# Optimization experiments

Hardware: AMD Instinct MI355X
Metric: run time of the kernel (lower is better)

Reference implementation:

```python
import jax, jax.numpy as jnp
import numpy as np

B, N, D = 4, 512, 128
NEG = -1e9


def setup_inputs() -> dict:
    key = jax.random.key(0)
    ks = jax.random.split(key, 11)
    s = 1.0 / np.sqrt(D)
    inp = {
        "q": jax.random.normal(ks[0], (B, N, D), jnp.float32),
        "k": jax.random.normal(ks[1], (B, N, D), jnp.float32),
        "v": jax.random.normal(ks[2], (B, N, D), jnp.float32),
        "mask": jnp.ones((B, N), jnp.int32),
        # nn.Linear params: weight [out,in], bias [out]
        "Wq": jax.random.uniform(ks[3], (D, D), jnp.float32, -s, s),
        "bq": jax.random.uniform(ks[4], (D,), jnp.float32, -s, s),
        "Wk": jax.random.uniform(ks[5], (D, D), jnp.float32, -s, s),
        "bk": jax.random.uniform(ks[6], (D,), jnp.float32, -s, s),
        "Wv": jax.random.uniform(ks[7], (D, D), jnp.float32, -s, s),
        "bv": jax.random.uniform(ks[8], (D,), jnp.float32, -s, s),
        "Wo": jax.random.uniform(ks[9], (D, D), jnp.float32, -s, s),
        "bo": jax.random.uniform(ks[10], (D,), jnp.float32, -s, s),
    }
    return inp


def reference(q, k, v, mask, Wq, bq, Wk, bk, Wv, bv, Wo, bo):
    # linear projections (torch Linear: x @ W.T + b)
    qp = jnp.einsum('bnd,ed->bne', q, Wq) + bq
    kp = jnp.einsum('bnd,ed->bne', k, Wk) + bk
    vp = jnp.einsum('bnd,ed->bne', v, Wv) + bv
    # outer-product attention: scores [b, n, m, d]
    scores = jnp.einsum('bnd,bmd->bnmd', qp, kp)
    # mask [b, n] -> [b, n, 1, 1], fill masked positions with -1e9
    scores = jnp.where(mask[:, :, None, None] == 0, NEG, scores)
    # per-channel softmax over m (axis=2); dropout is a no-op at inference
    scores = jax.nn.softmax(scores, axis=2)
    out = jnp.einsum('bnmd,bmd->bnd', scores, vp)
    return jnp.einsum('bnd,ed->bne', out, Wo) + bo
```

## Files before the change

kernel.cpp:

```cpp
#include <hip/hip_runtime.h>

#define BB 4
#define NN 512
#define DD 128

static constexpr float LOG2E = 1.4426950408889634f;
#define EXP2F(x) __builtin_amdgcn_exp2f(x)

__global__ __launch_bounds__(256) void wtrans_kernel(
    const float* __restrict__ Wq, const float* __restrict__ Wk,
    const float* __restrict__ Wv, const float* __restrict__ Wo,
    float* __restrict__ WTp)
{
    const int l = blockIdx.x * 256 + threadIdx.x;
    const int t = l >> 14;
    const int e = (l >> 7) & (DD - 1);
    const int j = l & (DD - 1);
    const float* W = (t == 0) ? Wq : (t == 1) ? Wk : (t == 2) ? Wv : Wo;
    WTp[(t << 14) + (j >> 2) * (DD * 4) + e * 4 + (j & 3)] = W[e * DD + j];
}

__global__ __launch_bounds__(256) void proj_kernel(
    const float* __restrict__ q, const float* __restrict__ k,
    const float* __restrict__ v, const float* __restrict__ WTp,
    const float* __restrict__ bq, const float* __restrict__ bk,
    const float* __restrict__ bv, const int* __restrict__ mask,
    float* __restrict__ qpT, float* __restrict__ kpT, float* __restrict__ vpT)
{
    const int t   = blockIdx.y;
    const int e   = threadIdx.x & (DD - 1);
    const int sub = threadIdx.x >> 7;
    const int g0  = blockIdx.x * 8 + sub * 4;

    const float*  x    = (t == 0) ? q   : (t == 1) ? k   : v;
    const float4* wt4  = (const float4*)(WTp + (t << 14));
    const float*  bias = (t == 0) ? bq  : (t == 1) ? bk  : bv;
    float*        outp = (t == 0) ? qpT : (t == 1) ? kpT : vpT;

    const float4* x0 = (const float4*)(x + (g0 + 0) * DD);
    const float4* x1 = (const float4*)(x + (g0 + 1) * DD);
    const float4* x2 = (const float4*)(x + (g0 + 2) * DD);
    const float4* x3 = (const float4*)(x + (g0 + 3) * DD);

    float a0 = 0.f, a1 = 0.f, a2 = 0.f, a3 = 0.f;
    #pragma unroll 4
    for (int j4 = 0; j4 < DD / 4; ++j4) {
        const float4 w  = wt4[j4 * DD + e];
        const float4 r0 = x0[j4];
        const float4 r1 = x1[j4];
        const float4 r2 = x2[j4];
        const float4 r3 = x3[j4];
        a0 = fmaf(r0.x, w.x, fmaf(r0.y, w.y, fmaf(r0.z, w.z, fmaf(r0.w, w.w, a0))));
        a1 = fmaf(r1.x, w.x, fmaf(r1.y, w.y, fmaf(r1.z, w.z, fmaf(r1.w, w.w, a1))));
        a2 = fmaf(r2.x, w.x, fmaf(r2.y, w.y, fmaf(r2.z, w.z, fmaf(r2.w, w.w, a2))));
        a3 = fmaf(r3.x, w.x, fmaf(r3.y, w.y, fmaf(r3.z, w.z, fmaf(r3.w, w.w, a3))));
    }

    const float be = bias[e];
    float acc[4] = {a0, a1, a2, a3};
    #pragma unroll
    for (int r = 0; r < 4; ++r) {
        const int g = g0 + r;
        const int b = g >> 9, n = g & (NN - 1);
        float val = acc[r] + be;
        if (t == 0) val = (mask[g] != 0) ? val * LOG2E : 0.f;
        outp[(b * DD + e) * NN + n] = val;
    }
}

__global__ __launch_bounds__(512) void attn_kernel(
    const float* __restrict__ qpT, const float* __restrict__ kpT,
    const float* __restrict__ vpT, float* __restrict__ att)
{
    __shared__ float sk[NN];
    __shared__ float sv[NN];
    __shared__ float pn[8][NN];
    __shared__ float pd[8][NN];

    const int bd  = blockIdx.x;
    const int b   = bd >> 7;
    const int d   = bd & (DD - 1);
    const int tid = threadIdx.x;
    const int h   = tid >> 6;
    const int i   = tid & 63;

    sk[tid] = kpT[bd * NN + tid];
    sv[tid] = vpT[bd * NN + tid];

    float qv[8];
    #pragma unroll
    for (int j = 0; j < 8; ++j)
        qv[j] = qpT[bd * NN + i + j * 64];
    __syncthreads();

    const float4* kc = (const float4*)sk;
    const float4* vc = (const float4*)sv;

    float na[8], da[8];
    #pragma unroll
    for (int j = 0; j < 8; ++j) { na[j] = 0.f; da[j] = 0.f; }

    const int m4lo = h * 16;
    #pragma unroll 2
    for (int m4 = m4lo; m4 < m4lo + 16; ++m4) {
        const float4 k4 = kc[m4];
        const float4 v4 = vc[m4];
        #pragma unroll
        for (int j = 0; j < 8; ++j) {
            const float p0 = EXP2F(qv[j] * k4.x);
            const float p1 = EXP2F(qv[j] * k4.y);
            const float p2 = EXP2F(qv[j] * k4.z);
            const float p3 = EXP2F(qv[j] * k4.w);
            na[j] = fmaf(p0, v4.x, na[j]);
            na[j] = fmaf(p1, v4.y, na[j]);
            na[j] = fmaf(p2, v4.z, na[j]);
            na[j] = fmaf(p3, v4.w, na[j]);
            da[j] += (p0 + p1) + (p2 + p3);
        }
    }

    #pragma unroll
    for (int j = 0; j < 8; ++j) {
        pn[h][i + j * 64] = na[j];
        pd[h][i + j * 64] = da[j];
    }
    __syncthreads();

    float num = 0.f, den = 0.f;
    #pragma unroll
    for (int hh = 0; hh < 8; ++hh) {
        num += pn[hh][tid];
        den += pd[hh][tid];
    }
    att[(b * NN + tid) * DD + d] = num / den;
}

__global__ __launch_bounds__(512) void outproj_kernel(
    const float* __restrict__ att, const float* __restrict__ WTp,
    const float* __restrict__ bo, float* __restrict__ out)
{
    const int e   = threadIdx.x & (DD - 1);
    const int sub = threadIdx.x >> 7;
    const int g   = blockIdx.x * 4 + sub;

    const float4* wt4 = (const float4*)(WTp + (3 << 14));
    const float4* xr  = (const float4*)(att + g * DD);

    float acc = 0.f;
    #pragma unroll 8
    for (int j4 = 0; j4 < DD / 4; ++j4) {
        const float4 w = wt4[j4 * DD + e];
        const float4 a = xr[j4];
        acc = fmaf(a.x, w.x, fmaf(a.y, w.y, fmaf(a.z, w.z, fmaf(a.w, w.w, acc))));
    }

    out[g * DD + e] = acc + bo[e];
}

extern "C" void kernel_launch(void* const* d_in, const int* in_sizes, int n_in,
                              void* d_out, int out_size, void* d_ws, size_t ws_size,
                              hipStream_t stream)
{
    const float* q    = (const float*)d_in[0];
    const float* k    = (const float*)d_in[1];
    const float* v    = (const float*)d_in[2];
    const int*   mask = (const int*)  d_in[3];
    const float* Wq   = (const float*)d_in[4];
    const float* bq   = (const float*)d_in[5];
    const float* Wk   = (const float*)d_in[6];
    const float* bk   = (const float*)d_in[7];
    const float* Wv   = (const float*)d_in[8];
    const float* bv   = (const float*)d_in[9];
    const float* Wo   = (const float*)d_in[10];
    const float* bo   = (const float*)d_in[11];
    float* out = (float*)d_out;

    float* ws  = (float*)d_ws;
    float* qpT = ws;
    float* kpT = ws + 1 * BB * DD * NN;
    float* vpT = ws + 2 * BB * DD * NN;
    float* att = ws + 3 * BB * DD * NN;
    float* WTp = ws + 4 * BB * DD * NN;

    wtrans_kernel<<<4 * DD * DD / 256, 256, 0, stream>>>(Wq, Wk, Wv, Wo, WTp);

    dim3 pgrid(BB * NN / 8, 3);
    proj_kernel<<<pgrid, 256, 0, stream>>>(q, k, v, WTp, bq, bk, bv, mask,
                                           qpT, kpT, vpT);

    attn_kernel<<<BB * DD, 512, 0, stream>>>(qpT, kpT, vpT, att);

    outproj_kernel<<<BB * NN / 4, 512, 0, stream>>>(att, WTp, bo, out);
}
```

Baseline: 126.1 us.

## Drop weight transpose kernel; stage transposed weights in LDS per block

Removes the separate weight-transpose kernel launch. The projection and output-projection kernels now load W directly into padded shared memory in transposed float4 layout. Projection blocks compute 8 rows per thread instead of 4, which halves the grid. The output projection uses 256-thread blocks with 2 rows per thread. This saves one launch and a global round trip, at the cost of each block re-reading the full 64KB weight into LDS, which limits occupancy.

```diff
diff --git a/kernel.cpp b/kernel.cpp
--- a/kernel.cpp
+++ b/kernel.cpp
@@ -7,61 +7,52 @@
 static constexpr float LOG2E = 1.4426950408889634f;
 #define EXP2F(x) __builtin_amdgcn_exp2f(x)
 
-__global__ __launch_bounds__(256) void wtrans_kernel(
-    const float* __restrict__ Wq, const float* __restrict__ Wk,
-    const float* __restrict__ Wv, const float* __restrict__ Wo,
-    float* __restrict__ WTp)
-{
-    const int l = blockIdx.x * 256 + threadIdx.x;
-    const int t = l >> 14;
-    const int e = (l >> 7) & (DD - 1);
-    const int j = l & (DD - 1);
-    const float* W = (t == 0) ? Wq : (t == 1) ? Wk : (t == 2) ? Wv : Wo;
-    WTp[(t << 14) + (j >> 2) * (DD * 4) + e * 4 + (j & 3)] = W[e * DD + j];
-}
-
 __global__ __launch_bounds__(256) void proj_kernel(
     const float* __restrict__ q, const float* __restrict__ k,
-    const float* __restrict__ v, const float* __restrict__ WTp,
-    const float* __restrict__ bq, const float* __restrict__ bk,
-    const float* __restrict__ bv, const int* __restrict__ mask,
+    const float* __restrict__ v, const int* __restrict__ mask,
+    const float* __restrict__ Wq, const float* __restrict__ bq,
+    const float* __restrict__ Wk, const float* __restrict__ bk,
+    const float* __restrict__ Wv, const float* __restrict__ bv,
     float* __restrict__ qpT, float* __restrict__ kpT, float* __restrict__ vpT)
 {
+    __shared__ float4 sW[32 * 129];
+
+    const int tid = threadIdx.x;
     const int t   = blockIdx.y;
-    const int e   = threadIdx.x & (DD - 1);
-    const int sub = threadIdx.x >> 7;
-    const int g0  = blockIdx.x * 8 + sub * 4;
+    const float4* W4 = (const float4*)((t == 0) ? Wq : (t == 1) ? Wk : Wv);
 
-    const float*  x    = (t == 0) ? q   : (t == 1) ? k   : v;
-    const float4* wt4  = (const float4*)(WTp + (t << 14));
-    const float*  bias = (t == 0) ? bq  : (t == 1) ? bk  : bv;
-    float*        outp = (t == 0) ? qpT : (t == 1) ? kpT : vpT;
+    #pragma unroll
+    for (int p = 0; p < 16; ++p) {
+        const int f = p * 256 + tid;
+        sW[(f & 31) * 129 + (f >> 5)] = W4[f];
+    }
+    __syncthreads();
 
-    const float4* x0 = (const float4*)(x + (g0 + 0) * DD);
-    const float4* x1 = (const float4*)(x + (g0 + 1) * DD);
-    const float4* x2 = (const float4*)(x + (g0 + 2) * DD);
-    const float4* x3 = (const float4*)(x + (g0 + 3) * DD);
+    const int e   = tid & 127;
+    const int sub = tid >> 7;
+    const int r0  = blockIdx.x * 16 + sub * 8;
+    const float* x    = (t == 0) ? q   : (t == 1) ? k   : v;
+    const float* bias = (t == 0) ? bq  : (t == 1) ? bk  : bv;
+    float*       outp = (t == 0) ? qpT : (t == 1) ? kpT : vpT;
 
-    float a0 = 0.f, a1 = 0.f, a2 = 0.f, a3 = 0.f;
+    float acc[8] = {0.f, 0.f, 0.f, 0.f, 0.f, 0.f, 0.f, 0.f};
     #pragma unroll 4
-    for (int j4 = 0; j4 < DD / 4; ++j4) {
-        const float4 w  = wt4[j4 * DD + e];
-        const float4 r0 = x0[j4];
-        const float4 r1 = x1[j4];
-        const float4 r2 = x2[j4];
-        const float4 r3 = x3[j4];
-        a0 = fmaf(r0.x, w.x, fmaf(r0.y, w.y, fmaf(r0.z, w.z, fmaf(r0.w, w.w, a0))));
-        a1 = fmaf(r1.x, w.x, fmaf(r1.y, w.y, fmaf(r1.z, w.z, fmaf(r1.w, w.w, a1))));
-        a2 = fmaf(r2.x, w.x, fmaf(r2.y, w.y, fmaf(r2.z, w.z, fmaf(r2.w, w.w, a2))));
-        a3 = fmaf(r3.x, w.x, fmaf(r3.y, w.y, fmaf(r3.z, w.z, fmaf(r3.w, w.w, a3))));
+    for (int j4 = 0; j4 < 32; ++j4) {
+        const float4 w = sW[j4 * 129 + e];
+        #pragma unroll
+        for (int r = 0; r < 8; ++r) {
+            const float4 xr = ((const float4*)(x + (r0 + r) * DD))[j4];
+            acc[r] = fmaf(xr.x, w.x, fmaf(xr.y, w.y,
+                     fmaf(xr.z, w.z, fmaf(xr.w, w.w, acc[r]))));
+        }
     }
 
     const float be = bias[e];
-    float acc[4] = {a0, a1, a2, a3};
+    const int b = r0 >> 9;
     #pragma unroll
-    for (int r = 0; r < 4; ++r) {
-        const int g = g0 + r;
-        const int b = g >> 9, n = g & (NN - 1);
+    for (int r = 0; r < 8; ++r) {
+        const int g = r0 + r;
+        const int n = g & (NN - 1);
         float val = acc[r] + be;
         if (t == 0) val = (mask[g] != 0) ? val * LOG2E : 0.f;
         outp[(b * DD + e) * NN + n] = val;
@@ -135,26 +126,41 @@
     att[(b * NN + tid) * DD + d] = num / den;
 }
 
-__global__ __launch_bounds__(512) void outproj_kernel(
-    const float* __restrict__ att, const float* __restrict__ WTp,
+__global__ __launch_bounds__(256) void outproj_kernel(
+    const float* __restrict__ att, const float* __restrict__ Wo,
     const float* __restrict__ bo, float* __restrict__ out)
 {
-    const int e   = threadIdx.x & (DD - 1);
-    const int sub = threadIdx.x >> 7;
-    const int g   = blockIdx.x * 4 + sub;
+    __shared__ float4 sW[32 * 129];
 
-    const float4* wt4 = (const float4*)(WTp + (3 << 14));
-    const float4* xr  = (const float4*)(att + g * DD);
+    const int tid = threadIdx.x;
+    const float4* Wo4 = (const float4*)Wo;
+    #pragma unroll
+    for (int p = 0; p < 16; ++p) {
+        const int f = p * 256 + tid;
+        sW[(f & 31) * 129 + (f >> 5)] = Wo4[f];
+    }
+    __syncthreads();
 
-    float acc = 0.f;
-    #pragma unroll 8
-    for (int j4 = 0; j4 < DD / 4; ++j4) {
-        const float4 w = wt4[j4 * DD + e];
-        const float4 a = xr[j4];
-        acc = fmaf(a.x, w.x, fmaf(a.y, w.y, fmaf(a.z, w.z, fmaf(a.w, w.w, acc))));
+    const int e   = tid & 127;
+    const int sub = tid >> 7;
+    const int g0  = blockIdx.x * 4 + sub * 2;
+
+    const float4* x0 = (const float4*)(att + g0 * DD);
+    const float4* x1 = (const float4*)(att + (g0 + 1) * DD);
+
+    float a0 = 0.f, a1 = 0.f;
+    #pragma unroll 4
+    for (int j4 = 0; j4 < 32; ++j4) {
+        const float4 w  = sW[j4 * 129 + e];
+        const float4 r0 = x0[j4];
+        const float4 r1 = x1[j4];
+        a0 = fmaf(r0.x, w.x, fmaf(r0.y, w.y, fmaf(r0.z, w.z, fmaf(r0.w, w.w, a0))));
+        a1 = fmaf(r1.x, w.x, fmaf(r1.y, w.y, fmaf(r1.z, w.z, fmaf(r1.w, w.w, a1))));
     }
 
-    out[g * DD + e] = acc + bo[e];
+    const float boe = bo[e];
+    out[(g0    ) * DD + e] = a0 + boe;
+    out[(g0 + 1) * DD + e] = a1 + boe;
 }
 
 extern "C" void kernel_launch(void* const* d_in, const int* in_sizes, int n_in,
@@ -180,15 +186,12 @@
     float* kpT = ws + 1 * BB * DD * NN;
     float* vpT = ws + 2 * BB * DD * NN;
     float* att = ws + 3 * BB * DD * NN;
-    float* WTp = ws + 4 * BB * DD * NN;
 
-    wtrans_kernel<<<4 * DD * DD / 256, 256, 0, stream>>>(Wq, Wk, Wv, Wo, WTp);
-
-    dim3 pgrid(BB * NN / 8, 3);
-    proj_kernel<<<pgrid, 256, 0, stream>>>(q, k, v, WTp, bq, bk, bv, mask,
-                                           qpT, kpT, vpT);
+    dim3 pgrid(BB * NN / 16, 3);
+    proj_kernel<<<pgrid, 256, 0, stream>>>(q, k, v, mask, Wq, bq, Wk, bk,
+                                           Wv, bv, qpT, kpT, vpT);
 
     attn_kernel<<<BB * DD, 512, 0, stream>>>(qpT, kpT, vpT, att);
 
-    outproj_kernel<<<BB * NN / 4, 512, 0, stream>>>(att, WTp, bo, out);
+    outproj_kernel<<<BB * NN / 4, 256, 0, stream>>>(att, Wo, bo, out);
 }
```

New measurement: 120.9 us. 4.1% less time.
